# Kernel tuning notes

Hardware: AMD Instinct MI355X
Metric: run time of the kernel (lower is better)

The kernel has to match this reference:

```python
import jax, jax.numpy as jnp
import numpy as np

N_NODES = 50000


def gcn_conv(x, src, dst, norm, W, b):
    # x: [N, Fin] -> linear transform then normalized scatter-add aggregation
    h = x @ W  # [N, Fout]
    msg = h[src] * norm[:, None]  # [E', Fout] gather + scale
    out = jax.ops.segment_sum(msg, dst, num_segments=N_NODES)  # scatter-add
    return out + b


def _build_graph(edge_index):
    # add self-loops (PyG GCNConv default) and compute symmetric normalization
    n = N_NODES
    loops = jnp.arange(n, dtype=edge_index.dtype)
    src = jnp.concatenate([edge_index[0], loops])
    dst = jnp.concatenate([edge_index[1], loops])
    deg = jax.ops.segment_sum(jnp.ones_like(dst, dtype=jnp.float32), dst, num_segments=n)
    dinv = jnp.where(deg > 0, jax.lax.rsqrt(deg), 0.0)
    norm = dinv[src] * dinv[dst]  # [E+N]
    return src, dst, norm


def setup_inputs() -> dict:
    key = jax.random.key(0)
    ks = jax.random.split(key, 8)
    in_c, out_c = 128, 64
    hid = 2 * out_c
    n_edges = 800000
    x = jax.random.normal(ks[0], (N_NODES, in_c), dtype=jnp.float32)
    edge_index = jax.random.randint(ks[1], (2, n_edges), 0, N_NODES, dtype=jnp.int64)
    s = 1.0 / np.sqrt(in_c)
    W1 = jax.random.uniform(ks[2], (in_c, hid), minval=-s, maxval=s, dtype=jnp.float32)
    b1 = jnp.zeros((hid,), dtype=jnp.float32)
    s2 = 1.0 / np.sqrt(hid)
    W_mu = jax.random.uniform(ks[3], (hid, out_c), minval=-s2, maxval=s2, dtype=jnp.float32)
    b_mu = jnp.zeros((out_c,), dtype=jnp.float32)
    W_ls = jax.random.uniform(ks[4], (hid, out_c), minval=-s2, maxval=s2, dtype=jnp.float32)
    b_ls = jnp.zeros((out_c,), dtype=jnp.float32)
    return {"x": x, "edge_index": edge_index, "W1": W1, "b1": b1,
            "W_mu": W_mu, "b_mu": b_mu, "W_ls": W_ls, "b_ls": b_ls}


def reference(x, edge_index, W1, b1, W_mu, b_mu, W_ls, b_ls):
    src, dst, norm = _build_graph(edge_index)
    h = jax.nn.relu(gcn_conv(x, src, dst, norm, W1, b1))
    mu = gcn_conv(h, src, dst, norm, W_mu, b_mu)
    logstd = gcn_conv(h, src, dst, norm, W_ls, b_ls)
    return mu, logstd
```

## Files before the change

kernel.cpp:

```cpp
#include <hip/hip_runtime.h>

#define N_NODES 50000
#define NE      800000
#define FDIM    128
#define OUTC    64
#define CAP     64

typedef _Float16 half4 __attribute__((ext_vector_type(4)));
typedef _Float16 f16x8 __attribute__((ext_vector_type(8)));
typedef float    f32x4 __attribute__((ext_vector_type(4)));



__global__ __launch_bounds__(256) void k_prep(int4* __restrict__ deg4,
                                              const float* __restrict__ W1,
                                              const float* __restrict__ Wmu,
                                              const float* __restrict__ Wls,
                                              const float* __restrict__ bmu,
                                              const float* __restrict__ bls,
                                              _Float16* __restrict__ W1T,
                                              _Float16* __restrict__ WoT,
                                              float* __restrict__ bo) {
    int b = blockIdx.x, tid = threadIdx.x;
    if (b < 49) {
        int i = b * 256 + tid;
        if (i < 12500) deg4[i] = make_int4(0, 0, 0, 0);
    } else {
        int j = (b - 49) * 256 + tid;
        if (j < 16384) {
            int n = j >> 7, k = j & 127;
            W1T[j] = (_Float16)W1[k * 128 + n];
        } else if (j < 32768) {
            int jj = j - 16384;
            int n = jj >> 7, k = jj & 127;
            WoT[jj] = (_Float16)(n < 64 ? Wmu[k * 64 + n] : Wls[k * 64 + (n - 64)]);
        } else if (j < 32896) {
            int n = j - 32768;
            bo[n] = (n < 64) ? bmu[n] : bls[n - 64];
        }
    }
}


__global__ __launch_bounds__(256) void k_count_fill(const int* __restrict__ ei,
                                                    int* __restrict__ deg,
                                                    int* __restrict__ pks) {
    int e = blockIdx.x * 256 + threadIdx.x;
    if (e < NE) {
        int s = ei[e];
        int d = ei[NE + e];
        int slot = atomicAdd(&deg[d], 1);
        if (slot < CAP) pks[d * CAP + slot] = s;
    }
}


__global__ __launch_bounds__(256) void k_scale(const float* __restrict__ x,
                                               const int* __restrict__ deg,
                                               float* __restrict__ dinv,
                                               _Float16* __restrict__ x16) {
    int i = blockIdx.x * 256 + threadIdx.x;
    if (i >= (N_NODES * FDIM) / 4) return;
    int node = i >> 5;
    float dv = rsqrtf((float)(deg[node] + 1));
    if ((i & 31) == 0) dinv[node] = dv;
    float4 v = reinterpret_cast<const float4*>(x)[i];
    half4 h = {(_Float16)(dv * v.x), (_Float16)(dv * v.y),
               (_Float16)(dv * v.z), (_Float16)(dv * v.w)};
    reinterpret_cast<half4*>(x16)[i] = h;
}


__device__ __forceinline__ void add4h(float4& a, half4 h) {
    a.x += (float)h.x; a.y += (float)h.y; a.z += (float)h.z; a.w += (float)h.w;
}

__device__ __forceinline__ void agg_tile(const _Float16* __restrict__ in,
                                         const int* __restrict__ pks,
                                         const int* __restrict__ deg,
                                         const float* __restrict__ dinv,
                                         _Float16 (*__restrict__ As)[136]) {
    int tid = threadIdx.x;
    int rl = tid >> 5;
    int r  = blockIdx.x * 16 + rl;
    int lane4 = (tid & 31) * 4;
    int cnt = deg[r]; if (cnt > CAP) cnt = CAP;
    const int* prow = pks + r * CAP;
    float4 a0 = {0,0,0,0}, a1 = {0,0,0,0}, a2 = {0,0,0,0}, a3 = {0,0,0,0};
    int e = 0;
    for (; e + 4 <= cnt; e += 4) {
        int s0 = prow[e], s1 = prow[e+1], s2 = prow[e+2], s3 = prow[e+3];
        add4h(a0, *reinterpret_cast<const half4*>(&in[(size_t)s0 * FDIM + lane4]));
        add4h(a1, *reinterpret_cast<const half4*>(&in[(size_t)s1 * FDIM + lane4]));
        add4h(a2, *reinterpret_cast<const half4*>(&in[(size_t)s2 * FDIM + lane4]));
        add4h(a3, *reinterpret_cast<const half4*>(&in[(size_t)s3 * FDIM + lane4]));
    }
    for (; e < cnt; ++e)
        add4h(a0, *reinterpret_cast<const half4*>(&in[(size_t)prow[e] * FDIM + lane4]));
    add4h(a1, *reinterpret_cast<const half4*>(&in[(size_t)r * FDIM + lane4]));
    float dv = dinv[r];
    half4 g = {(_Float16)(dv * ((a0.x + a1.x) + (a2.x + a3.x))),
               (_Float16)(dv * ((a0.y + a1.y) + (a2.y + a3.y))),
               (_Float16)(dv * ((a0.z + a1.z) + (a2.z + a3.z))),
               (_Float16)(dv * ((a0.w + a1.w) + (a2.w + a3.w)))};
    *reinterpret_cast<half4*>(&As[rl][lane4]) = g;
}


__global__ __launch_bounds__(512) void k_layer1(const _Float16* __restrict__ x16,
                                                const int* __restrict__ pks,
                                                const int* __restrict__ deg,
                                                const float* __restrict__ dinv,
                                                const _Float16* __restrict__ W1T,
                                                const float* __restrict__ b1,
                                                _Float16* __restrict__ H16) {
    __shared__ _Float16 As[16][136];
    agg_tile(x16, pks, deg, dinv, As);
    __syncthreads();
    int tid = threadIdx.x;
    int wave = tid >> 6, lane = tid & 63;
    int colg = lane & 15;
    int kg8 = (lane >> 4) * 8;
    f32x4 acc = {0.f, 0.f, 0.f, 0.f};
    #pragma unroll
    for (int ks = 0; ks < 4; ++ks) {
        f16x8 a  = *reinterpret_cast<const f16x8*>(&As[colg][ks * 32 + kg8]);
        f16x8 bf = *reinterpret_cast<const f16x8*>(
            &W1T[(size_t)(wave * 16 + colg) * FDIM + ks * 32 + kg8]);
        acc = __builtin_amdgcn_mfma_f32_16x16x32_f16(a, bf, acc, 0, 0, 0);
    }
    int col = wave * 16 + colg;
    float bias = b1[col];
    int r0 = (lane >> 4) * 4;
    #pragma unroll
    for (int r = 0; r < 4; ++r) {
        int m = blockIdx.x * 16 + r0 + r;
        float h = fmaxf(acc[r] + bias, 0.f);
        H16[(size_t)m * FDIM + col] = (_Float16)(dinv[m] * h);
    }
}

__global__ __launch_bounds__(512) void k_layer2(const _Float16* __restrict__ h16,
                                                const int* __restrict__ pks,
                                                const int* __restrict__ deg,
                                                const float* __restrict__ dinv,
                                                const _Float16* __restrict__ WoT,
                                                const float* __restrict__ bo,
                                                float* __restrict__ MU,
                                                float* __restrict__ LS) {
    __shared__ _Float16 As[16][136];
    agg_tile(h16, pks, deg, dinv, As);
    __syncthreads();
    int tid = threadIdx.x;
    int wave = tid >> 6, lane = tid & 63;
    int colg = lane & 15;
    int kg8 = (lane >> 4) * 8;
    f32x4 acc = {0.f, 0.f, 0.f, 0.f};
    #pragma unroll
    for (int ks = 0; ks < 4; ++ks) {
        f16x8 a  = *reinterpret_cast<const f16x8*>(&As[colg][ks * 32 + kg8]);
        f16x8 bf = *reinterpret_cast<const f16x8*>(
            &WoT[(size_t)(wave * 16 + colg) * FDIM + ks * 32 + kg8]);
        acc = __builtin_amdgcn_mfma_f32_16x16x32_f16(a, bf, acc, 0, 0, 0);
    }
    int col = wave * 16 + colg;
    float bias = bo[col];
    int r0 = (lane >> 4) * 4;
    #pragma unroll
    for (int r = 0; r < 4; ++r) {
        int m = blockIdx.x * 16 + r0 + r;
        float v = acc[r] + bias;
        if (col < 64) MU[(size_t)m * OUTC + col] = v;
        else          LS[(size_t)m * OUTC + (col - 64)] = v;
    }
}


extern "C" void kernel_launch(void* const* d_in, const int* in_sizes, int n_in,
                              void* d_out, int out_size, void* d_ws, size_t ws_size,
                              hipStream_t stream) {
    const float* x   = (const float*)d_in[0];
    const int*   ei  = (const int*)d_in[1];
    const float* W1  = (const float*)d_in[2];
    const float* b1  = (const float*)d_in[3];
    const float* Wmu = (const float*)d_in[4];
    const float* bmu = (const float*)d_in[5];
    const float* Wls = (const float*)d_in[6];
    const float* bls = (const float*)d_in[7];
    float* out = (float*)d_out;

    char* ws = (char*)d_ws;
    int*      deg  = (int*)     (ws + 0);
    float*    dinv = (float*)   (ws + 200000);
    int*      pks  = (int*)     (ws + 400000);
    _Float16* W1T  = (_Float16*)(ws + 13200000);
    _Float16* WoT  = (_Float16*)(ws + 13232768);
    float*    bo   = (float*)   (ws + 13265536);
    _Float16* h16  = (_Float16*)(ws + 13266048);

    _Float16* x16 = (_Float16*)d_out;

    k_prep      <<<49 + 129, 256, 0, stream>>>((int4*)deg, W1, Wmu, Wls, bmu, bls,
                                               W1T, WoT, bo);
    k_count_fill<<<(NE + 255) / 256, 256, 0, stream>>>(ei, deg, pks);
    k_scale     <<<(N_NODES * FDIM / 4 + 255) / 256, 256, 0, stream>>>(x, deg, dinv, x16);

    k_layer1<<<N_NODES / 16, 512, 0, stream>>>(x16, pks, deg, dinv, W1T, b1, h16);
    k_layer2<<<N_NODES / 16, 512, 0, stream>>>(h16, pks, deg, dinv, WoT, bo,
                                               out, out + (size_t)N_NODES * OUTC);
}
```

Measured before the change: 157.4 us.

## Split fused aggregate+GEMM into separate kernels and compress neighbor indices to 16-bit

Replaces the two fused aggregate-then-MFMA layer kernels with a standalone gather/aggregation kernel plus separate GEMM kernels. Each GEMM block now computes 64 rows by all 128 columns per wave, so weight loads are reused across eight MFMA tiles. The neighbor-list buffer switches from int32 to uint16, which halves index traffic and allows vectorized four-index loads. The cost is extra kernel launches and a round trip of the aggregated features through global memory. Node ids up to 49999 fit in 16 bits, so the narrowing stays correct for this graph size.

```diff
diff --git a/kernel.cpp b/kernel.cpp
--- a/kernel.cpp
+++ b/kernel.cpp
@@ -9,6 +9,7 @@
 typedef _Float16 half4 __attribute__((ext_vector_type(4)));
 typedef _Float16 f16x8 __attribute__((ext_vector_type(8)));
 typedef float    f32x4 __attribute__((ext_vector_type(4)));
+typedef unsigned short us4 __attribute__((ext_vector_type(4)));
 
 
 
@@ -44,13 +45,13 @@
 
 __global__ __launch_bounds__(256) void k_count_fill(const int* __restrict__ ei,
                                                     int* __restrict__ deg,
-                                                    int* __restrict__ pks) {
+                                                    unsigned short* __restrict__ pks) {
     int e = blockIdx.x * 256 + threadIdx.x;
     if (e < NE) {
         int s = ei[e];
         int d = ei[NE + e];
         int slot = atomicAdd(&deg[d], 1);
-        if (slot < CAP) pks[d * CAP + slot] = s;
+        if (slot < CAP) pks[d * CAP + slot] = (unsigned short)s;
     }
 }
 
@@ -75,103 +76,114 @@
     a.x += (float)h.x; a.y += (float)h.y; a.z += (float)h.z; a.w += (float)h.w;
 }
 
-__device__ __forceinline__ void agg_tile(const _Float16* __restrict__ in,
-                                         const int* __restrict__ pks,
-                                         const int* __restrict__ deg,
-                                         const float* __restrict__ dinv,
-                                         _Float16 (*__restrict__ As)[136]) {
+__global__ __launch_bounds__(256) void k_agg(const _Float16* __restrict__ in,
+                                             _Float16* __restrict__ out,
+                                             const unsigned short* __restrict__ pks,
+                                             const int* __restrict__ deg,
+                                             const float* __restrict__ dinv) {
     int tid = threadIdx.x;
-    int rl = tid >> 5;
-    int r  = blockIdx.x * 16 + rl;
+    int r = blockIdx.x * 8 + (tid >> 5);
+    if (r >= N_NODES) return;
     int lane4 = (tid & 31) * 4;
     int cnt = deg[r]; if (cnt > CAP) cnt = CAP;
-    const int* prow = pks + r * CAP;
+    const unsigned short* prow = pks + r * CAP;
     float4 a0 = {0,0,0,0}, a1 = {0,0,0,0}, a2 = {0,0,0,0}, a3 = {0,0,0,0};
     int e = 0;
     for (; e + 4 <= cnt; e += 4) {
-        int s0 = prow[e], s1 = prow[e+1], s2 = prow[e+2], s3 = prow[e+3];
-        add4h(a0, *reinterpret_cast<const half4*>(&in[(size_t)s0 * FDIM + lane4]));
-        add4h(a1, *reinterpret_cast<const half4*>(&in[(size_t)s1 * FDIM + lane4]));
-        add4h(a2, *reinterpret_cast<const half4*>(&in[(size_t)s2 * FDIM + lane4]));
-        add4h(a3, *reinterpret_cast<const half4*>(&in[(size_t)s3 * FDIM + lane4]));
+        us4 s4 = *reinterpret_cast<const us4*>(prow + e);
+        add4h(a0, *reinterpret_cast<const half4*>(&in[(size_t)s4[0] * FDIM + lane4]));
+        add4h(a1, *reinterpret_cast<const half4*>(&in[(size_t)s4[1] * FDIM + lane4]));
+        add4h(a2, *reinterpret_cast<const half4*>(&in[(size_t)s4[2] * FDIM + lane4]));
+        add4h(a3, *reinterpret_cast<const half4*>(&in[(size_t)s4[3] * FDIM + lane4]));
     }
     for (; e < cnt; ++e)
         add4h(a0, *reinterpret_cast<const half4*>(&in[(size_t)prow[e] * FDIM + lane4]));
     add4h(a1, *reinterpret_cast<const half4*>(&in[(size_t)r * FDIM + lane4]));
     float dv = dinv[r];
-    half4 g = {(_Float16)(dv * ((a0.x + a1.x) + (a2.x + a3.x))),
+    half4 o = {(_Float16)(dv * ((a0.x + a1.x) + (a2.x + a3.x))),
                (_Float16)(dv * ((a0.y + a1.y) + (a2.y + a3.y))),
                (_Float16)(dv * ((a0.z + a1.z) + (a2.z + a3.z))),
                (_Float16)(dv * ((a0.w + a1.w) + (a2.w + a3.w)))};
-    *reinterpret_cast<half4*>(&As[rl][lane4]) = g;
-}
-
-
-__global__ __launch_bounds__(512) void k_layer1(const _Float16* __restrict__ x16,
-                                                const int* __restrict__ pks,
-                                                const int* __restrict__ deg,
-                                                const float* __restrict__ dinv,
-                                                const _Float16* __restrict__ W1T,
-                                                const float* __restrict__ b1,
-                                                _Float16* __restrict__ H16) {
-    __shared__ _Float16 As[16][136];
-    agg_tile(x16, pks, deg, dinv, As);
-    __syncthreads();
+    *reinterpret_cast<half4*>(&out[(size_t)r * FDIM + lane4]) = o;
+}
+
+
+__global__ __launch_bounds__(256) void k_gemm1(const _Float16* __restrict__ A,
+                                               const _Float16* __restrict__ WT,
+                                               const float* __restrict__ b,
+                                               const float* __restrict__ dinv,
+                                               _Float16* __restrict__ H) {
     int tid = threadIdx.x;
     int wave = tid >> 6, lane = tid & 63;
-    int colg = lane & 15;
+    int m0 = blockIdx.x * 64 + wave * 16;
     int kg8 = (lane >> 4) * 8;
-    f32x4 acc = {0.f, 0.f, 0.f, 0.f};
+    const _Float16* Ap = A + (size_t)(m0 + (lane & 15)) * FDIM + kg8;
+    f32x4 acc[8];
+    #pragma unroll
+    for (int t = 0; t < 8; ++t) acc[t] = (f32x4){0.f, 0.f, 0.f, 0.f};
     #pragma unroll
     for (int ks = 0; ks < 4; ++ks) {
-        f16x8 a  = *reinterpret_cast<const f16x8*>(&As[colg][ks * 32 + kg8]);
-        f16x8 bf = *reinterpret_cast<const f16x8*>(
-            &W1T[(size_t)(wave * 16 + colg) * FDIM + ks * 32 + kg8]);
-        acc = __builtin_amdgcn_mfma_f32_16x16x32_f16(a, bf, acc, 0, 0, 0);
-    }
-    int col = wave * 16 + colg;
-    float bias = b1[col];
-    int r0 = (lane >> 4) * 4;
-    #pragma unroll
-    for (int r = 0; r < 4; ++r) {
-        int m = blockIdx.x * 16 + r0 + r;
-        float h = fmaxf(acc[r] + bias, 0.f);
-        H16[(size_t)m * FDIM + col] = (_Float16)(dinv[m] * h);
-    }
-}
-
-__global__ __launch_bounds__(512) void k_layer2(const _Float16* __restrict__ h16,
-                                                const int* __restrict__ pks,
-                                                const int* __restrict__ deg,
-                                                const float* __restrict__ dinv,
-                                                const _Float16* __restrict__ WoT,
-                                                const float* __restrict__ bo,
-                                                float* __restrict__ MU,
-                                                float* __restrict__ LS) {
-    __shared__ _Float16 As[16][136];
-    agg_tile(h16, pks, deg, dinv, As);
-    __syncthreads();
+        f16x8 a = *reinterpret_cast<const f16x8*>(Ap + ks * 32);
+        #pragma unroll
+        for (int t = 0; t < 8; ++t) {
+            f16x8 bf = *reinterpret_cast<const f16x8*>(
+                WT + (size_t)(t * 16 + (lane & 15)) * FDIM + ks * 32 + kg8);
+            acc[t] = __builtin_amdgcn_mfma_f32_16x16x32_f16(a, bf, acc[t], 0, 0, 0);
+        }
+    }
+    int rbase = m0 + ((lane >> 4) << 2);
+    #pragma unroll
+    for (int t = 0; t < 8; ++t) {
+        int col = t * 16 + (lane & 15);
+        float bias = b[col];
+        #pragma unroll
+        for (int r = 0; r < 4; ++r) {
+            int m = rbase + r;
+            if (m < N_NODES) {
+                float h = fmaxf(acc[t][r] + bias, 0.f);
+                H[(size_t)m * FDIM + col] = (_Float16)(dinv[m] * h);
+            }
+        }
+    }
+}
+
+__global__ __launch_bounds__(256) void k_gemm_out(const _Float16* __restrict__ A,
+                                                  const _Float16* __restrict__ WT,
+                                                  const float* __restrict__ bo,
+                                                  float* __restrict__ MU,
+                                                  float* __restrict__ LS) {
     int tid = threadIdx.x;
     int wave = tid >> 6, lane = tid & 63;
-    int colg = lane & 15;
+    int m0 = blockIdx.x * 64 + wave * 16;
     int kg8 = (lane >> 4) * 8;
-    f32x4 acc = {0.f, 0.f, 0.f, 0.f};
+    const _Float16* Ap = A + (size_t)(m0 + (lane & 15)) * FDIM + kg8;
+    f32x4 acc[8];
+    #pragma unroll
+    for (int t = 0; t < 8; ++t) acc[t] = (f32x4){0.f, 0.f, 0.f, 0.f};
     #pragma unroll
     for (int ks = 0; ks < 4; ++ks) {
-        f16x8 a  = *reinterpret_cast<const f16x8*>(&As[colg][ks * 32 + kg8]);
-        f16x8 bf = *reinterpret_cast<const f16x8*>(
-            &WoT[(size_t)(wave * 16 + colg) * FDIM + ks * 32 + kg8]);
-        acc = __builtin_amdgcn_mfma_f32_16x16x32_f16(a, bf, acc, 0, 0, 0);
-    }
-    int col = wave * 16 + colg;
-    float bias = bo[col];
-    int r0 = (lane >> 4) * 4;
-    #pragma unroll
-    for (int r = 0; r < 4; ++r) {
-        int m = blockIdx.x * 16 + r0 + r;
-        float v = acc[r] + bias;
-        if (col < 64) MU[(size_t)m * OUTC + col] = v;
-        else          LS[(size_t)m * OUTC + (col - 64)] = v;
+        f16x8 a = *reinterpret_cast<const f16x8*>(Ap + ks * 32);
+        #pragma unroll
+        for (int t = 0; t < 8; ++t) {
+            f16x8 bf = *reinterpret_cast<const f16x8*>(
+                WT + (size_t)(t * 16 + (lane & 15)) * FDIM + ks * 32 + kg8);
+            acc[t] = __builtin_amdgcn_mfma_f32_16x16x32_f16(a, bf, acc[t], 0, 0, 0);
+        }
+    }
+    int rbase = m0 + ((lane >> 4) << 2);
+    #pragma unroll
+    for (int t = 0; t < 8; ++t) {
+        int col = t * 16 + (lane & 15);
+        float bias = bo[col];
+        #pragma unroll
+        for (int r = 0; r < 4; ++r) {
+            int m = rbase + r;
+            if (m < N_NODES) {
+                float v = acc[t][r] + bias;
+                if (col < 64) MU[(size_t)m * OUTC + col] = v;
+                else          LS[(size_t)m * OUTC + (col - 64)] = v;
+            }
+        }
     }
 }
 
@@ -190,22 +202,25 @@
     float* out = (float*)d_out;
 
     char* ws = (char*)d_ws;
-    int*      deg  = (int*)     (ws + 0);
-    float*    dinv = (float*)   (ws + 200000);
-    int*      pks  = (int*)     (ws + 400000);
-    _Float16* W1T  = (_Float16*)(ws + 13200000);
-    _Float16* WoT  = (_Float16*)(ws + 13232768);
-    float*    bo   = (float*)   (ws + 13265536);
-    _Float16* h16  = (_Float16*)(ws + 13266048);
-
-    _Float16* x16 = (_Float16*)d_out;
+    int*            deg  = (int*)           (ws + 0);
+    float*          dinv = (float*)         (ws + 200000);
+    unsigned short* pks  = (unsigned short*)(ws + 400000);
+    _Float16*       W1T  = (_Float16*)      (ws + 6800000);
+    _Float16*       WoT  = (_Float16*)      (ws + 6832768);
+    float*          bo   = (float*)         (ws + 6865536);
+    _Float16*       g16  = (_Float16*)      (ws + 6866048);
+
+    _Float16* f16buf = (_Float16*)d_out;
 
     k_prep      <<<49 + 129, 256, 0, stream>>>((int4*)deg, W1, Wmu, Wls, bmu, bls,
                                                W1T, WoT, bo);
     k_count_fill<<<(NE + 255) / 256, 256, 0, stream>>>(ei, deg, pks);
-    k_scale     <<<(N_NODES * FDIM / 4 + 255) / 256, 256, 0, stream>>>(x, deg, dinv, x16);
-
-    k_layer1<<<N_NODES / 16, 512, 0, stream>>>(x16, pks, deg, dinv, W1T, b1, h16);
-    k_layer2<<<N_NODES / 16, 512, 0, stream>>>(h16, pks, deg, dinv, WoT, bo,
-                                               out, out + (size_t)N_NODES * OUTC);
-}
+    k_scale     <<<(N_NODES * FDIM / 4 + 255) / 256, 256, 0, stream>>>(x, deg, dinv, f16buf);
+
+    k_agg  <<<(N_NODES + 7) / 8, 256, 0, stream>>>(f16buf, g16, pks, deg, dinv);
+    k_gemm1<<<(N_NODES + 63) / 64, 256, 0, stream>>>(g16, W1T, b1, dinv, f16buf);
+
+    k_agg     <<<(N_NODES + 7) / 8, 256, 0, stream>>>(f16buf, g16, pks, deg, dinv);
+    k_gemm_out<<<(N_NODES + 63) / 64, 256, 0, stream>>>(g16, WoT, bo,
+                                                        out, out + (size_t)N_NODES * OUTC);
+}
```

Result: slower. 179.6 us (+14.1%).
